# Optimization experiments

Hardware: AMD Instinct MI355X
Metric: run time of the kernel (lower is better)

The kernel has to match this reference:

```python
import jax, jax.numpy as jnp
import numpy as np
from jax import lax

KERNELS = (3, 5, 7, 9, 11, 13, 15)
H = W = 4096


def _box_mean(x, k):
    """2D box-mean filter with replicate (edge) padding, computed separably.

    Edge padding is separable, so (pad2d -> kxk box) == (padH -> kx1 box -> padW -> 1xk box).
    x: [N, 1, H, W]
    """
    p = k // 2
    kh = jnp.full((1, 1, k, 1), 1.0 / k, dtype=x.dtype)
    kw = jnp.full((1, 1, 1, k), 1.0 / k, dtype=x.dtype)
    dn = ('NCHW', 'OIHW', 'NCHW')
    y = jnp.pad(x, ((0, 0), (0, 0), (p, p), (0, 0)), mode='edge')
    y = lax.conv_general_dilated(y, kh, (1, 1), 'VALID', dimension_numbers=dn)
    y = jnp.pad(y, ((0, 0), (0, 0), (0, 0), (p, p)), mode='edge')
    y = lax.conv_general_dilated(y, kw, (1, 1), 'VALID', dimension_numbers=dn)
    return y


def setup_inputs() -> dict:
    key = jax.random.key(0)
    k1, k2 = jax.random.split(key)
    x = jax.random.uniform(k1, (1, 1, H, W), dtype=jnp.float32)
    # binary occupancy-style map, as float (torch uses mapU8 -> fp16 multiply)
    map_mask = (jax.random.uniform(k2, (H, W)) > 0.5).astype(jnp.float32)
    return {"x": x, "map_mask": map_mask}


def reference(x, map_mask):
    # sum of 7 multi-scale box means, averaged, then masked by the map
    acc = _box_mean(x, KERNELS[0])
    for k in KERNELS[1:]:
        acc = acc + _box_mean(x, k)
    out = acc / len(KERNELS)
    return out * map_mask[None, None, :, :]
```

## Files before the change

### kernel.cpp

```cpp
#include <hip/hip_runtime.h>


#define TILE   64
#define HALO   7
#define LHX    8
#define NCOL   80
#define NROW   78
#define PSTR   83
#define PROWSA 81
#define HH     4096
#define WW     4096

__global__ __launch_bounds__(256) void meanconv_kernel(
    const float* __restrict__ x, const float* __restrict__ mask,
    float* __restrict__ out)
{
    __shared__ float P[PROWSA * PSTR];
    const int tid    = threadIdx.x;
    const int c0     = blockIdx.x * TILE;
    const int r0base = blockIdx.y * (2 * TILE);

    if (tid < 81) P[tid] = 0.0f;

    const bool xint = (c0 >= LHX) && (c0 - LHX + NCOL <= WW);

    auto load_seg = [&](int r0, int idx, float* v) {
        const int lr  = idx >> 2;
        const int s   = idx & 3;
        const int gr  = min(max(r0 + lr - HALO, 0), HH - 1);
        const int gc0 = c0 - LHX + 20 * s;
        if (xint) {
            const float* src = &x[(size_t)gr * WW + gc0];
            #pragma unroll
            for (int q = 0; q < 5; ++q) {
                const float4 t = *(const float4*)(src + 4 * q);
                v[4*q+0] = t.x; v[4*q+1] = t.y; v[4*q+2] = t.z; v[4*q+3] = t.w;
            }
        } else {
            #pragma unroll
            for (int i = 0; i < 20; ++i) {
                const int gc = min(max(gc0 + i, 0), WW - 1);
                v[i] = x[(size_t)gr * WW + gc];
            }
        }
    };
    auto prefix_write = [&](int idx, float* v) {
        const int lr = idx >> 2;
        const int s  = idx & 3;
        #pragma unroll
        for (int i = 1; i < 20; ++i) v[i] += v[i - 1];
        const float tot = v[19];
        float sum = tot;
        float u = __shfl_up(sum, 1, 4); if (s >= 1) sum += u;
        u       = __shfl_up(sum, 2, 4); if (s >= 2) sum += u;
        const float off = sum - tot;
        float* dst = &P[(lr + 1) * PSTR + 1 + 20 * s];
        #pragma unroll
        for (int i = 0; i < 20; ++i) dst[i] = v[i] + off;
    };

    const int g  = tid & 3;
    const int ty = tid >> 2;
    const int B0 = 16 * g;
    const int A  = ty + HALO;

    float v[20];
    load_seg(r0base, tid, v);

    #pragma unroll
    for (int t = 0; t < 2; ++t) {
        const int r0 = r0base + TILE * t;

        prefix_write(tid, v);
        if (tid < 56) {
            float w2[20];
            load_seg(r0, tid + 256, w2);
            prefix_write(tid + 256, w2);
        }
        __syncthreads();

        for (int idx = tid; idx < 80 * 4; idx += 256) {
            const int c  = (idx >> 2) + 1;
            const int s  = idx & 3;
            const int rs = 1 + 20 * s;
            float vv[20];
            float run = 0.0f;
            #pragma unroll
            for (int i = 0; i < 20; ++i) {
                const int r = rs + i;
                float tt = P[r * PSTR + c];
                tt = (r < 79) ? tt : 0.0f;
                run += tt; vv[i] = run;
            }
            const float tot = run;
            float sum = tot;
            float u = __shfl_up(sum, 1, 4); if (s >= 1) sum += u;
            u       = __shfl_up(sum, 2, 4); if (s >= 2) sum += u;
            const float off = sum - tot;
            #pragma unroll
            for (int i = 0; i < 20; ++i) {
                const int r = rs + i;
                if (r < 79) P[r * PSTR + c] = vv[i] + off;
            }
        }
        __syncthreads();

        if (t == 0) load_seg(r0base + TILE, tid, v);

        const int gr = r0 + ty, gc = c0 + B0;
        const float* mrow = &mask[(size_t)gr * WW + gc];
        const float4 m0 = *(const float4*)(mrow);
        const float4 m1 = *(const float4*)(mrow + 4);
        const float4 m2 = *(const float4*)(mrow + 8);
        const float4 m3 = *(const float4*)(mrow + 12);

        float a[16];
        #pragma unroll
        for (int i = 0; i < 16; ++i) a[i] = 0.0f;

        #pragma unroll
        for (int p = 1; p <= 7; ++p) {
            const int   k = 2 * p + 1;
            const float wgt = 1.0f / (7.0f * (float)(k * k));
            const int   W = 17 + 2 * p;
            const float* rT = &P[(A - p)     * PSTR + B0 + LHX - p];
            const float* rB = &P[(A + p + 1) * PSTR + B0 + LHX - p];
            float D[31];
            #pragma unroll
            for (int q = 0; q < W; ++q) D[q] = rB[q] - rT[q];
            #pragma unroll
            for (int i = 0; i < 16; ++i)
                a[i] += wgt * (D[k + i] - D[i]);
        }
        __syncthreads();

        float* orow = &out[(size_t)gr * WW + gc];
        float4 o;
        o.x = a[0]*m0.x;  o.y = a[1]*m0.y;  o.z = a[2]*m0.z;  o.w = a[3]*m0.w;
        *(float4*)(orow)      = o;
        o.x = a[4]*m1.x;  o.y = a[5]*m1.y;  o.z = a[6]*m1.z;  o.w = a[7]*m1.w;
        *(float4*)(orow + 4)  = o;
        o.x = a[8]*m2.x;  o.y = a[9]*m2.y;  o.z = a[10]*m2.z; o.w = a[11]*m2.w;
        *(float4*)(orow + 8)  = o;
        o.x = a[12]*m3.x; o.y = a[13]*m3.y; o.z = a[14]*m3.z; o.w = a[15]*m3.w;
        *(float4*)(orow + 12) = o;
    }
}

extern "C" void kernel_launch(void* const* d_in, const int* in_sizes, int n_in,
                              void* d_out, int out_size, void* d_ws, size_t ws_size,
                              hipStream_t stream) {
    const float* x    = (const float*)d_in[0];
    const float* mask = (const float*)d_in[1];
    float*       out  = (float*)d_out;
    dim3 grid(WW / TILE, HH / (2 * TILE));
    meanconv_kernel<<<grid, 256, 0, stream>>>(x, mask, out);
}
```

Before: 194.1 us.

## Prefetch second tile's input into LDS via async global_load_lds

Replaces the register-held prefetch of the next tile's rows with an asynchronous global-to-LDS copy (global_load_lds) into a new 25.6KB shared buffer XS, issued before the box-sum compute of the first tile. The second tile's row-prefix pass then reads from LDS instead of global memory. The goal is to cut register pressure and overlap the global load latency with compute. It also moves the mask load to after the compute and drops the final barrier in the second iteration. In exchange, the larger shared-memory footprint may lower occupancy, and the async copy relies on the barrier for visibility.

```diff
diff --git a/kernel.cpp b/kernel.cpp
--- a/kernel.cpp
+++ b/kernel.cpp
@@ -1,4 +1,5 @@
 #include <hip/hip_runtime.h>
+#include <stdint.h>
 
 
 #define TILE   64
@@ -10,12 +11,15 @@
 #define PROWSA 81
 #define HH     4096
 #define WW     4096
+#define XSTR   80
+#define XCHUNK 25
 
 __global__ __launch_bounds__(256) void meanconv_kernel(
     const float* __restrict__ x, const float* __restrict__ mask,
     float* __restrict__ out)
 {
     __shared__ float P[PROWSA * PSTR];
+    __shared__ float XS[XCHUNK * 256];
     const int tid    = threadIdx.x;
     const int c0     = blockIdx.x * TILE;
     const int r0base = blockIdx.y * (2 * TILE);
@@ -24,39 +28,49 @@
 
     const bool xint = (c0 >= LHX) && (c0 - LHX + NCOL <= WW);
 
-    auto load_seg = [&](int r0, int idx, float* v) {
-        const int lr  = idx >> 2;
-        const int s   = idx & 3;
-        const int gr  = min(max(r0 + lr - HALO, 0), HH - 1);
-        const int gc0 = c0 - LHX + 20 * s;
-        if (xint) {
-            const float* src = &x[(size_t)gr * WW + gc0];
+    auto p1_pass = [&](int r0, int mode) {
+        for (int idx = tid; idx < NROW * 4; idx += 256) {
+            const int lr = idx >> 2;
+            const int s  = idx & 3;
+            float v[20];
+            if (mode == 1) {
+                const float* sr = &XS[lr * XSTR + 20 * s];
+                #pragma unroll
+                for (int q = 0; q < 5; ++q) {
+                    const float4 t4 = *(const float4*)(sr + 4 * q);
+                    v[4*q+0] = t4.x; v[4*q+1] = t4.y;
+                    v[4*q+2] = t4.z; v[4*q+3] = t4.w;
+                }
+            } else {
+                const int gr  = min(max(r0 + lr - HALO, 0), HH - 1);
+                const int gc0 = c0 - LHX + 20 * s;
+                if (xint) {
+                    const float* src = &x[(size_t)gr * WW + gc0];
+                    #pragma unroll
+                    for (int q = 0; q < 5; ++q) {
+                        const float4 t4 = *(const float4*)(src + 4 * q);
+                        v[4*q+0] = t4.x; v[4*q+1] = t4.y;
+                        v[4*q+2] = t4.z; v[4*q+3] = t4.w;
+                    }
+                } else {
+                    #pragma unroll
+                    for (int i = 0; i < 20; ++i) {
+                        const int gc = min(max(gc0 + i, 0), WW - 1);
+                        v[i] = x[(size_t)gr * WW + gc];
+                    }
+                }
+            }
             #pragma unroll
-            for (int q = 0; q < 5; ++q) {
-                const float4 t = *(const float4*)(src + 4 * q);
-                v[4*q+0] = t.x; v[4*q+1] = t.y; v[4*q+2] = t.z; v[4*q+3] = t.w;
-            }
-        } else {
+            for (int i = 1; i < 20; ++i) v[i] += v[i - 1];
+            const float tot = v[19];
+            float sum = tot;
+            float u = __shfl_up(sum, 1, 4); if (s >= 1) sum += u;
+            u       = __shfl_up(sum, 2, 4); if (s >= 2) sum += u;
+            const float off = sum - tot;
+            float* dst = &P[(lr + 1) * PSTR + 1 + 20 * s];
             #pragma unroll
-            for (int i = 0; i < 20; ++i) {
-                const int gc = min(max(gc0 + i, 0), WW - 1);
-                v[i] = x[(size_t)gr * WW + gc];
-            }
+            for (int i = 0; i < 20; ++i) dst[i] = v[i] + off;
         }
-    };
-    auto prefix_write = [&](int idx, float* v) {
-        const int lr = idx >> 2;
-        const int s  = idx & 3;
-        #pragma unroll
-        for (int i = 1; i < 20; ++i) v[i] += v[i - 1];
-        const float tot = v[19];
-        float sum = tot;
-        float u = __shfl_up(sum, 1, 4); if (s >= 1) sum += u;
-        u       = __shfl_up(sum, 2, 4); if (s >= 2) sum += u;
-        const float off = sum - tot;
-        float* dst = &P[(lr + 1) * PSTR + 1 + 20 * s];
-        #pragma unroll
-        for (int i = 0; i < 20; ++i) dst[i] = v[i] + off;
     };
 
     const int g  = tid & 3;
@@ -64,19 +78,12 @@
     const int B0 = 16 * g;
     const int A  = ty + HALO;
 
-    float v[20];
-    load_seg(r0base, tid, v);
-
-    #pragma unroll
     for (int t = 0; t < 2; ++t) {
         const int r0 = r0base + TILE * t;
 
-        prefix_write(tid, v);
-        if (tid < 56) {
-            float w2[20];
-            load_seg(r0, tid + 256, w2);
-            prefix_write(tid + 256, w2);
-        }
+        if (t == 0)      p1_pass(r0, 0);
+        else if (xint)   p1_pass(r0, 1);
+        else             p1_pass(r0, 0);
         __syncthreads();
 
         for (int idx = tid; idx < 80 * 4; idx += 256) {
@@ -105,24 +112,29 @@
         }
         __syncthreads();
 
-        if (t == 0) load_seg(r0base + TILE, tid, v);
-
-        const int gr = r0 + ty, gc = c0 + B0;
-        const float* mrow = &mask[(size_t)gr * WW + gc];
-        const float4 m0 = *(const float4*)(mrow);
-        const float4 m1 = *(const float4*)(mrow + 4);
-        const float4 m2 = *(const float4*)(mrow + 8);
-        const float4 m3 = *(const float4*)(mrow + 12);
+        if (t == 0 && xint) {
+            const int wv = tid >> 6, ln = tid & 63;
+            const int r1 = r0base + TILE;
+            for (int ch = wv; ch < XCHUNK; ch += 4) {
+                const int u_  = ch * 64 + ln;
+                const int row = u_ / 20;
+                const int c4  = u_ - row * 20;
+                const int gr  = min(max(r1 + row - HALO, 0), HH - 1);
+                const float* src = &x[(size_t)gr * WW + (c0 - LHX + 4 * c4)];
+                float* dst = &XS[ch * 256];
+                __builtin_amdgcn_global_load_lds(
+                    (const uint32_t*)src, (uint32_t*)dst, 16, 0, 0);
+            }
+        }
 
         float a[16];
         #pragma unroll
         for (int i = 0; i < 16; ++i) a[i] = 0.0f;
-
         #pragma unroll
         for (int p = 1; p <= 7; ++p) {
-            const int   k = 2 * p + 1;
+            const int   k   = 2 * p + 1;
             const float wgt = 1.0f / (7.0f * (float)(k * k));
-            const int   W = 17 + 2 * p;
+            const int   W   = 17 + 2 * p;
             const float* rT = &P[(A - p)     * PSTR + B0 + LHX - p];
             const float* rB = &P[(A + p + 1) * PSTR + B0 + LHX - p];
             float D[31];
@@ -132,18 +144,21 @@
             for (int i = 0; i < 16; ++i)
                 a[i] += wgt * (D[k + i] - D[i]);
         }
-        __syncthreads();
+        if (t == 0) __syncthreads();
 
-        float* orow = &out[(size_t)gr * WW + gc];
-        float4 o;
-        o.x = a[0]*m0.x;  o.y = a[1]*m0.y;  o.z = a[2]*m0.z;  o.w = a[3]*m0.w;
-        *(float4*)(orow)      = o;
-        o.x = a[4]*m1.x;  o.y = a[5]*m1.y;  o.z = a[6]*m1.z;  o.w = a[7]*m1.w;
-        *(float4*)(orow + 4)  = o;
-        o.x = a[8]*m2.x;  o.y = a[9]*m2.y;  o.z = a[10]*m2.z; o.w = a[11]*m2.w;
-        *(float4*)(orow + 8)  = o;
-        o.x = a[12]*m3.x; o.y = a[13]*m3.y; o.z = a[14]*m3.z; o.w = a[15]*m3.w;
-        *(float4*)(orow + 12) = o;
+        const int gr = r0 + ty, gc = c0 + B0;
+        const float* mrow = &mask[(size_t)gr * WW + gc];
+        float*       orow = &out[(size_t)gr * WW + gc];
+        #pragma unroll
+        for (int q = 0; q < 4; ++q) {
+            const float4 m = *(const float4*)(mrow + 4 * q);
+            float4 o4;
+            o4.x = a[4*q+0] * m.x;
+            o4.y = a[4*q+1] * m.y;
+            o4.z = a[4*q+2] * m.z;
+            o4.w = a[4*q+3] * m.w;
+            *(float4*)(orow + 4 * q) = o4;
+        }
     }
 }
 
```

Result: slower. 259.0 us (+33.4%).
